# Optimization experiments

Measured on AMD Instinct MI355X. Metric: run time of the kernel, lower is better.

The kernel has to match this reference:

```python
import jax, jax.numpy as jnp
import numpy as np

N_EMBED = 1024
HEAD_SIZE = 128
B, T = 8, 2048


def setup_inputs() -> dict:
    key = jax.random.key(0)
    kx, kk, kq, kv = jax.random.split(key, 4)
    x = jax.random.normal(kx, (B, T, N_EMBED), dtype=jnp.float32)
    Wk = jax.random.normal(kk, (N_EMBED, HEAD_SIZE), dtype=jnp.float32) * (N_EMBED ** -0.5)
    Wq = jax.random.normal(kq, (N_EMBED, HEAD_SIZE), dtype=jnp.float32) * (N_EMBED ** -0.5)
    Wv = jax.random.normal(kv, (N_EMBED, HEAD_SIZE), dtype=jnp.float32) * (N_EMBED ** -0.5)
    return {"x": x, "Wk": Wk, "Wq": Wq, "Wv": Wv}


def reference(x, Wk, Wq, Wv):
    # x: [B, T, C]; single-head causal attention, dropout rate 0 (identity)
    t = x.shape[1]
    k = jnp.einsum("btc,ch->bth", x, Wk)  # keys
    q = jnp.einsum("btc,ch->bth", x, Wq)  # queries
    v = jnp.einsum("btc,ch->bth", x, Wv)  # values
    scale = k.shape[-1] ** -0.5
    scores = jnp.einsum("bqh,bkh->bqk", q, k) * scale  # [B, T, T]
    causal = jnp.tril(jnp.ones((t, t), dtype=bool))
    scores = jnp.where(causal, scores, -jnp.inf)
    attn = jax.nn.softmax(scores, axis=-1)
    return jnp.einsum("bqk,bkh->bqh", attn, v)
```

## Files before the change

### kernel.cpp

```cpp
#include <hip/hip_runtime.h>
#include <hip/hip_bf16.h>
#include <math.h>

#define B_ 8
#define T_ 2048
#define C_ 1024
#define D_ 128
#define M_ (B_*T_)

typedef __attribute__((ext_vector_type(8))) short short8;
typedef __attribute__((ext_vector_type(4))) float floatx4;
typedef __hip_bfloat16 bf16;

#define QSCALE 0.12751744416218247f

#define GLDS16(gsrc, ldst) \
    __builtin_amdgcn_global_load_lds((const __attribute__((address_space(1))) unsigned int*)(gsrc), \
                                     (__attribute__((address_space(3))) unsigned int*)(ldst), 16, 0, 0)

__global__ __launch_bounds__(256) void cvt_w3_kernel(const float* __restrict__ Wq,
                                                     const float* __restrict__ Wk,
                                                     const float* __restrict__ Wv,
                                                     bf16* __restrict__ Wt2) {
    __shared__ bf16 tl[64][136];
    const int t = threadIdx.x;
    const int kc = blockIdx.x, g = blockIdx.y;
    const int k0 = kc * 64;
    const float* W = (g == 0) ? Wq : (g == 1) ? Wk : Wv;
    {
        int k = t >> 2, n0 = (t & 3) * 32;
        const float* src = W + (size_t)(k0 + k) * 128 + n0;
#pragma unroll
        for (int j = 0; j < 4; ++j) {
            float4 v0 = *(const float4*)(src + j * 8);
            float4 v1 = *(const float4*)(src + j * 8 + 4);
            union { short8 s; __hip_bfloat162 h[4]; } u;
            __hip_bfloat162 h;
            h.x = __float2bfloat16(v0.x); h.y = __float2bfloat16(v0.y); u.h[0] = h;
            h.x = __float2bfloat16(v0.z); h.y = __float2bfloat16(v0.w); u.h[1] = h;
            h.x = __float2bfloat16(v1.x); h.y = __float2bfloat16(v1.y); u.h[2] = h;
            h.x = __float2bfloat16(v1.z); h.y = __float2bfloat16(v1.w); u.h[3] = h;
            *(short8*)&tl[k][n0 + j * 8] = u.s;
        }
    }
    __syncthreads();
    {
#pragma unroll
        for (int j = 0; j < 4; ++j) {
            int cid = t + j * 256;
            int lane = cid & 63, dk = (cid >> 6) & 1, cb = cid >> 7;
            int krow = dk * 32 + (lane >> 4) * 8;
            int ncol = cb * 16 + (lane & 15);
            union { short8 s; bf16 e[8]; } u;
#pragma unroll
            for (int e = 0; e < 8; ++e) u.e[e] = tl[krow + e][ncol];
            bf16* dst = Wt2 + ((((size_t)(g * 8 + cb) * 16 + kc) * 2 + dk) * 64 + lane) * 8;
            *(short8*)dst = u.s;
        }
    }
}

__global__ __launch_bounds__(256, 2) void proj13_kernel(const float* __restrict__ x,
                                                        const bf16* __restrict__ Wt2,
                                                        bf16* __restrict__ Qb,
                                                        bf16* __restrict__ Kb,
                                                        bf16* __restrict__ Vt) {
    __shared__ char smem[57344];
    bf16* wlds = (bf16*)smem;
    const int t = threadIdx.x;
    const int wave = t >> 6, lane = t & 63;
    const int quad = lane >> 4, l15 = lane & 15;
    const int wr = wave >> 1, wc = wave & 1;
    const int phys = blockIdx.x;
    const int lb = (phys & 7) * 64 + (phys >> 3);
    const int rt = lb >> 1, cg = lb & 1;
    const int row0 = rt * 64;

    const float* xsrc[4];
#pragma unroll
    for (int j = 0; j < 4; ++j)
        xsrc[j] = x + (size_t)(row0 + (wave * 4 + j) * 4 + quad) * 1024
                    + 4 * ((lane & 15) ^ ((j & 1) * 4 + quad));

    const bf16* wsrc[6];
#pragma unroll
    for (int j = 0; j < 6; ++j) {
        const int s = j * 4 + wave;
        const int chunkbase = (cg * 12 + (s >> 1)) * 32 + (s & 1);
        wsrc[j] = Wt2 + (size_t)chunkbase * 512 + lane * 8;
    }

    floatx4 acc[2][6];
#pragma unroll
    for (int m = 0; m < 2; ++m)
#pragma unroll
        for (int n = 0; n < 6; ++n) acc[m][n] = (floatx4)0.0f;

#pragma unroll
    for (int j = 0; j < 4; ++j)
        GLDS16(xsrc[j], smem + 24576 + (wave * 4 + j) * 1024);

    for (int kc = 0; kc < 16; ++kc) {
        __syncthreads();
#pragma unroll
        for (int j = 0; j < 6; ++j) {
            const int s = j * 4 + wave;
            GLDS16(wsrc[j] + kc * 1024, smem + s * 1024);
        }
        __syncthreads();
        if (kc < 15) {
            char* xd = smem + 24576 + ((kc + 1) & 1) * 16384;
#pragma unroll
            for (int j = 0; j < 4; ++j)
                GLDS16(xsrc[j] + (kc + 1) * 64, xd + (wave * 4 + j) * 1024);
        }
        const float* xb = (const float*)(smem + 24576 + (kc & 1) * 16384);
#pragma unroll
        for (int dk = 0; dk < 2; ++dk) {
            short8 af[2], bff[6];
#pragma unroll
            for (int m = 0; m < 2; ++m) {
                const int r = wr * 32 + m * 16 + l15;
                const int p0 = (dk * 32 + quad * 8) ^ ((l15 & 7) * 4);
                float4 a0 = *(const float4*)(xb + r * 64 + p0);
                float4 a1 = *(const float4*)(xb + r * 64 + (p0 ^ 4));
                union { short8 s; __hip_bfloat162 h[4]; } u;
                __hip_bfloat162 hh;
                hh.x = __float2bfloat16(a0.x); hh.y = __float2bfloat16(a0.y); u.h[0] = hh;
                hh.x = __float2bfloat16(a0.z); hh.y = __float2bfloat16(a0.w); u.h[1] = hh;
                hh.x = __float2bfloat16(a1.x); hh.y = __float2bfloat16(a1.y); u.h[2] = hh;
                hh.x = __float2bfloat16(a1.z); hh.y = __float2bfloat16(a1.w); u.h[3] = hh;
                af[m] = u.s;
            }
#pragma unroll
            for (int n = 0; n < 6; ++n) {
                const int c = wc * 6 + n;
                bff[n] = *(const short8*)(wlds + (size_t)(c * 2 + dk) * 512 + lane * 8);
            }
#pragma unroll
            for (int m = 0; m < 2; ++m)
#pragma unroll
                for (int n = 0; n < 6; ++n)
                    acc[m][n] = __builtin_amdgcn_mfma_f32_16x16x32_bf16(af[m], bff[n], acc[m][n], 0, 0, 0);
        }
    }

    __syncthreads();
    bf16* vtl = (bf16*)smem;
#pragma unroll
    for (int m = 0; m < 2; ++m)
#pragma unroll
        for (int r = 0; r < 4; ++r) {
            const int tt = wr * 32 + m * 16 + quad * 4 + r;
            const int row = row0 + tt;
#pragma unroll
            for (int n = 0; n < 6; ++n) {
                const int colb = cg * 192 + wc * 96 + n * 16;
                const int g = colb >> 7;
                const int lc = (colb & 127) + l15;
                const float v = acc[m][n][r];
                if (g == 0)      Qb[(size_t)row * 128 + lc] = __float2bfloat16(v * QSCALE);
                else if (g == 1) Kb[(size_t)row * 128 + lc] = __float2bfloat16(v);
                else             vtl[tt * 137 + lc] = __float2bfloat16(v);
            }
        }
    if (cg == 1) {
        __syncthreads();
        int d = t >> 1, toff = (t & 1) * 32;
        union { short8 s[4]; bf16 e[32]; } u;
#pragma unroll
        for (int i = 0; i < 32; ++i) u.e[i] = vtl[(toff + i) * 137 + d];
        int bb = row0 >> 11, t0 = row0 & 2047;
        bf16* dst = Vt + (size_t)(bb * D_ + d) * T_ + t0 + toff;
#pragma unroll
        for (int j = 0; j < 4; ++j) *(short8*)(dst + j * 8) = u.s[j];
    }
}

__global__ __launch_bounds__(256, 3) void flash_fm2_kernel(const bf16* __restrict__ Qb,
                                                           const bf16* __restrict__ Kb,
                                                           const bf16* __restrict__ Vt,
                                                           float* __restrict__ out,
                                                           bf16* __restrict__ Opart,
                                                           float* __restrict__ Lpart) {
    const int tile = blockIdx.x, seg = blockIdx.y, b = blockIdx.z;
    const int keys_total = (tile + 1) * 64;
    const int nseg = (keys_total + 255) >> 8;
    if (seg >= nseg) return;

    __shared__ bf16 lds_k[64][136];
    __shared__ bf16 lds_v[128][72];
    __shared__ bf16 lds_p[4][16][72];
    const int t = threadIdx.x;
    const int wave = t >> 6, lane = t & 63;
    const int quad = lane >> 4, l15 = lane & 15;
    const int q0 = tile * 64;
    const int k_start = seg << 8;
    const int k_end = min(k_start + 256, keys_total);
    const int nch = (k_end - k_start) >> 6;

    short8 qf[4];
    {
        int qm = q0 + wave * 16 + l15;
#pragma unroll
        for (int dk = 0; dk < 4; ++dk)
            qf[dk] = *(const short8*)(Qb + (size_t)(b * T_ + qm) * 128 + dk * 32 + quad * 8);
    }

    short8 kreg[4], vreg[4];
    {
        const int k0 = k_start;
#pragma unroll
        for (int j = 0; j < 4; ++j) {
            int c = t + j * 256;
            { int r = c >> 4, co = (c & 15) * 8;
              kreg[j] = *(const short8*)(Kb + (size_t)(b * T_ + k0 + r) * 128 + co); }
            { int d = c >> 3, co = (c & 7) * 8;
              vreg[j] = *(const short8*)(Vt + (size_t)b * (D_ * T_) + d * T_ + k0 + co); }
        }
    }

    floatx4 o_acc[8];
#pragma unroll
    for (int i = 0; i < 8; ++i) o_acc[i] = (floatx4)0.0f;
    float lp[4] = {0.f, 0.f, 0.f, 0.f};
    const int qrow = q0 + wave * 16 + quad * 4;

    for (int ch = 0; ch < nch; ++ch) {
        const int k0 = k_start + (ch << 6);
        __syncthreads();
#pragma unroll
        for (int j = 0; j < 4; ++j) {
            int c = t + j * 256;
            { int r = c >> 4, co = (c & 15) * 8; *(short8*)&lds_k[r][co] = kreg[j]; }
            { int d = c >> 3, co = (c & 7) * 8;  *(short8*)&lds_v[d][co] = vreg[j]; }
        }
        if (ch + 1 < nch) {
            const int kn = k0 + 64;
#pragma unroll
            for (int j = 0; j < 4; ++j) {
                int c = t + j * 256;
                { int r = c >> 4, co = (c & 15) * 8;
                  kreg[j] = *(const short8*)(Kb + (size_t)(b * T_ + kn + r) * 128 + co); }
                { int d = c >> 3, co = (c & 7) * 8;
                  vreg[j] = *(const short8*)(Vt + (size_t)b * (D_ * T_) + d * T_ + kn + co); }
            }
        }
        __syncthreads();

        floatx4 s[4];
#pragma unroll
        for (int nt = 0; nt < 4; ++nt) s[nt] = (floatx4)0.0f;
#pragma unroll
        for (int dk = 0; dk < 4; ++dk)
#pragma unroll
            for (int nt = 0; nt < 4; ++nt) {
                short8 kb = *(const short8*)&lds_k[nt * 16 + l15][dk * 32 + quad * 8];
                s[nt] = __builtin_amdgcn_mfma_f32_16x16x32_bf16(qf[dk], kb, s[nt], 0, 0, 0);
            }

        float sv[4][4];
#pragma unroll
        for (int nt = 0; nt < 4; ++nt)
#pragma unroll
            for (int r = 0; r < 4; ++r) sv[nt][r] = s[nt][r];

        if (k0 + 63 > q0) {
#pragma unroll
            for (int nt = 0; nt < 4; ++nt) {
                int key = k0 + nt * 16 + l15;
#pragma unroll
                for (int r = 0; r < 4; ++r)
                    if (key > qrow + r) sv[nt][r] = -1e30f;
            }
        }

#pragma unroll
        for (int nt = 0; nt < 4; ++nt)
#pragma unroll
            for (int r = 0; r < 4; ++r) sv[nt][r] = exp2f(sv[nt][r]);
#pragma unroll
        for (int r = 0; r < 4; ++r)
            lp[r] += (sv[0][r] + sv[1][r]) + (sv[2][r] + sv[3][r]);

#pragma unroll
        for (int nt = 0; nt < 4; ++nt)
#pragma unroll
            for (int r = 0; r < 4; ++r)
                lds_p[wave][quad * 4 + r][nt * 16 + l15] = __float2bfloat16(sv[nt][r]);
        short8 pa0 = *(const short8*)&lds_p[wave][l15][quad * 8];
        short8 pa1 = *(const short8*)&lds_p[wave][l15][32 + quad * 8];

#pragma unroll
        for (int nt = 0; nt < 8; ++nt) {
            short8 vb0 = *(const short8*)&lds_v[nt * 16 + l15][quad * 8];
            short8 vb1 = *(const short8*)&lds_v[nt * 16 + l15][32 + quad * 8];
            o_acc[nt] = __builtin_amdgcn_mfma_f32_16x16x32_bf16(pa0, vb0, o_acc[nt], 0, 0, 0);
            o_acc[nt] = __builtin_amdgcn_mfma_f32_16x16x32_bf16(pa1, vb1, o_acc[nt], 0, 0, 0);
        }
    }

    float l_i[4];
#pragma unroll
    for (int r = 0; r < 4; ++r) {
        float v = lp[r];
        v += __shfl_xor(v, 1);
        v += __shfl_xor(v, 2);
        v += __shfl_xor(v, 4);
        v += __shfl_xor(v, 8);
        l_i[r] = v;
    }

    const int lrow = wave * 16 + quad * 4;
    if (nseg == 1) {
        float inv_l[4];
#pragma unroll
        for (int r = 0; r < 4; ++r) inv_l[r] = 1.0f / l_i[r];
#pragma unroll
        for (int f = 0; f < 8; ++f)
#pragma unroll
            for (int r = 0; r < 4; ++r)
                out[(size_t)(b * T_ + qrow + r) * 128 + f * 16 + l15] = o_acc[f][r] * inv_l[r];
    } else {
        int pre = 0;
        for (int u = 4; u < tile; ++u) pre += (u + 4) >> 2;
        const size_t slot = (size_t)b * 140 + pre + seg;
        bf16* ob = Opart + slot * (64 * 128);
#pragma unroll
        for (int f = 0; f < 8; ++f)
#pragma unroll
            for (int r = 0; r < 4; ++r)
                ob[(size_t)(lrow + r) * 128 + f * 16 + l15] = __float2bfloat16(o_acc[f][r]);
        if (l15 == 0) {
#pragma unroll
            for (int r = 0; r < 4; ++r)
                Lpart[slot * 64 + lrow + r] = l_i[r];
        }
    }
}

__global__ __launch_bounds__(256) void combine4_kernel(const bf16* __restrict__ Opart,
                                                       const float* __restrict__ Lpart,
                                                       float* __restrict__ out) {
    const int tile = blockIdx.x + 4, b = blockIdx.y;
    const int nseg = (tile + 4) >> 2;
    int pre = 0;
    for (int u = 4; u < tile; ++u) pre += (u + 4) >> 2;
    const size_t slot0 = (size_t)b * 140 + pre;
    const int t = threadIdx.x;
    const int row = t >> 2, c0 = (t & 3) * 32;

    float lsum = 0.f;
    for (int j = 0; j < nseg; ++j) lsum += Lpart[(slot0 + j) * 64 + row];

    float acc[32];
#pragma unroll
    for (int i = 0; i < 32; ++i) acc[i] = 0.f;
    for (int j = 0; j < nseg; ++j) {
        const bf16* src = Opart + (slot0 + j) * (64 * 128) + (size_t)row * 128 + c0;
#pragma unroll
        for (int u = 0; u < 4; ++u) {
            short8 v8 = *(const short8*)(src + u * 8);
#pragma unroll
            for (int e = 0; e < 8; ++e) {
                union { unsigned int u32; float f; } cv;
                cv.u32 = ((unsigned int)(unsigned short)v8[e]) << 16;
                acc[u * 8 + e] += cv.f;
            }
        }
    }
    float inv = 1.0f / lsum;
    float* dst = out + (size_t)(b * T_ + tile * 64 + row) * 128 + c0;
#pragma unroll
    for (int i = 0; i < 32; ++i) dst[i] = acc[i] * inv;
}

extern "C" void kernel_launch(void* const* d_in, const int* in_sizes, int n_in,
                              void* d_out, int out_size, void* d_ws, size_t ws_size,
                              hipStream_t stream) {
    const float* x  = (const float*)d_in[0];
    const float* Wk = (const float*)d_in[1];
    const float* Wq = (const float*)d_in[2];
    const float* Wv = (const float*)d_in[3];
    float* out = (float*)d_out;

    char* ws = (char*)d_ws;
    bf16*  Wt2   = (bf16*)ws;
    bf16*  Qb    = (bf16*)(ws + 786432);
    bf16*  Kb    = (bf16*)(ws + 4980736);
    bf16*  Vt    = (bf16*)(ws + 9175040);
    bf16*  Opart = (bf16*)(ws + 13369344);
    float* Lpart = (float*)(ws + 31719424);

    cvt_w3_kernel<<<dim3(16, 3), 256, 0, stream>>>(Wq, Wk, Wv, Wt2);
    proj13_kernel<<<512, 256, 0, stream>>>(x, Wt2, Qb, Kb, Vt);
    flash_fm2_kernel<<<dim3(32, 8, B_), 256, 0, stream>>>(Qb, Kb, Vt, out, Opart, Lpart);
    combine4_kernel<<<dim3(28, B_), 256, 0, stream>>>(Opart, Lpart, out);
}
```

Baseline: 84.33 us.

## Convert x to bf16 once via registers and double-buffer weight tiles in projection

The projection kernel now loads x fp32 tiles into registers, converts them to bf16 once and stores them swizzled into LDS, instead of staging fp32 via global_load_lds and converting on every MFMA operand read. Weight tiles become double-buffered, with one barrier pair per k-chunk and explicit waitcnt/sched_barrier control, so the next chunk's loads overlap the current chunk's MFMAs. This cuts repeated conversion work and the LDS footprint of x. In exchange it raises LDS to 64KB, which may limit occupancy at two blocks per CU, and adds register pressure from prefetching x.

```diff
diff --git a/kernel.cpp b/kernel.cpp
--- a/kernel.cpp
+++ b/kernel.cpp
@@ -60,13 +60,12 @@
     }
 }
 
-__global__ __launch_bounds__(256, 2) void proj13_kernel(const float* __restrict__ x,
+__global__ __launch_bounds__(256, 2) void proj14_kernel(const float* __restrict__ x,
                                                         const bf16* __restrict__ Wt2,
                                                         bf16* __restrict__ Qb,
                                                         bf16* __restrict__ Kb,
                                                         bf16* __restrict__ Vt) {
-    __shared__ char smem[57344];
-    bf16* wlds = (bf16*)smem;
+    __shared__ __attribute__((aligned(16))) char smem[65536];
     const int t = threadIdx.x;
     const int wave = t >> 6, lane = t & 63;
     const int quad = lane >> 4, l15 = lane & 15;
@@ -76,12 +75,6 @@
     const int rt = lb >> 1, cg = lb & 1;
     const int row0 = rt * 64;
 
-    const float* xsrc[4];
-#pragma unroll
-    for (int j = 0; j < 4; ++j)
-        xsrc[j] = x + (size_t)(row0 + (wave * 4 + j) * 4 + quad) * 1024
-                    + 4 * ((lane & 15) ^ ((j & 1) * 4 + quad));
-
     const bf16* wsrc[6];
 #pragma unroll
     for (int j = 0; j < 6; ++j) {
@@ -90,60 +83,98 @@
         wsrc[j] = Wt2 + (size_t)chunkbase * 512 + lane * 8;
     }
 
+    const int xwrow = t >> 2;
+    const float* xbase = x + (size_t)(row0 + xwrow) * 1024 + (t & 3) * 16;
+    const int xwb0 = xwrow * 128 + (((t & 3) * 32) ^ ((xwrow & 7) << 4));
+    const int xwb1 = xwrow * 128 + ((((t & 3) * 32) + 16) ^ ((xwrow & 7) << 4));
+
     floatx4 acc[2][6];
 #pragma unroll
     for (int m = 0; m < 2; ++m)
 #pragma unroll
         for (int n = 0; n < 6; ++n) acc[m][n] = (floatx4)0.0f;
 
-#pragma unroll
-    for (int j = 0; j < 4; ++j)
-        GLDS16(xsrc[j], smem + 24576 + (wave * 4 + j) * 1024);
-
-    for (int kc = 0; kc < 16; ++kc) {
-        __syncthreads();
-#pragma unroll
-        for (int j = 0; j < 6; ++j) {
-            const int s = j * 4 + wave;
-            GLDS16(wsrc[j] + kc * 1024, smem + s * 1024);
-        }
-        __syncthreads();
-        if (kc < 15) {
-            char* xd = smem + 24576 + ((kc + 1) & 1) * 16384;
+    float4 xr[4];
+
+#define CVT_STORE_X(dstbase)                                                          \
+    {                                                                                 \
+        union { short8 s; __hip_bfloat162 h[4]; } u0, u1;                             \
+        __hip_bfloat162 h;                                                            \
+        h.x = __float2bfloat16(xr[0].x); h.y = __float2bfloat16(xr[0].y); u0.h[0] = h;\
+        h.x = __float2bfloat16(xr[0].z); h.y = __float2bfloat16(xr[0].w); u0.h[1] = h;\
+        h.x = __float2bfloat16(xr[1].x); h.y = __float2bfloat16(xr[1].y); u0.h[2] = h;\
+        h.x = __float2bfloat16(xr[1].z); h.y = __float2bfloat16(xr[1].w); u0.h[3] = h;\
+        h.x = __float2bfloat16(xr[2].x); h.y = __float2bfloat16(xr[2].y); u1.h[0] = h;\
+        h.x = __float2bfloat16(xr[2].z); h.y = __float2bfloat16(xr[2].w); u1.h[1] = h;\
+        h.x = __float2bfloat16(xr[3].x); h.y = __float2bfloat16(xr[3].y); u1.h[2] = h;\
+        h.x = __float2bfloat16(xr[3].z); h.y = __float2bfloat16(xr[3].w); u1.h[3] = h;\
+        *(short8*)((dstbase) + xwb0) = u0.s;                                          \
+        *(short8*)((dstbase) + xwb1) = u1.s;                                          \
+    }
+
+#define COMPUTE_KC(kc_)                                                               \
+    {                                                                                 \
+        const char* xb = smem + 49152 + ((kc_) & 1) * 8192;                           \
+        const char* wb = smem + ((kc_) & 1) * 24576;                                  \
+        _Pragma("unroll")                                                             \
+        for (int dk = 0; dk < 2; ++dk) {                                              \
+            short8 af[2], bff[6];                                                     \
+            _Pragma("unroll")                                                         \
+            for (int m = 0; m < 2; ++m) {                                             \
+                const int row = wr * 32 + m * 16 + l15;                               \
+                const int byt = row * 128 + ((dk * 64 + quad * 16) ^ ((row & 7) << 4));\
+                af[m] = *(const short8*)(xb + byt);                                   \
+            }                                                                         \
+            _Pragma("unroll")                                                         \
+            for (int n = 0; n < 6; ++n)                                               \
+                bff[n] = *(const short8*)(wb + (size_t)((wc * 6 + n) * 2 + dk) * 1024 \
+                                           + lane * 16);                              \
+            _Pragma("unroll")                                                         \
+            for (int m = 0; m < 2; ++m)                                               \
+                _Pragma("unroll")                                                     \
+                for (int n = 0; n < 6; ++n)                                           \
+                    acc[m][n] = __builtin_amdgcn_mfma_f32_16x16x32_bf16(af[m], bff[n],\
+                                                                  acc[m][n], 0, 0, 0);\
+        }                                                                             \
+    }
+
+#pragma unroll
+    for (int j = 0; j < 4; ++j) xr[j] = *(const float4*)(xbase + j * 4);
+    CVT_STORE_X(smem + 49152)
+#pragma unroll
+    for (int j = 0; j < 6; ++j)
+        GLDS16(wsrc[j], smem + (j * 4 + wave) * 1024);
+#pragma unroll
+    for (int j = 0; j < 4; ++j) xr[j] = *(const float4*)(xbase + 64 + j * 4);
+
+    for (int kc = 0; kc < 15; ++kc) {
+        __builtin_amdgcn_s_barrier();
+        {
+            char* wdst = smem + ((kc + 1) & 1) * 24576;
+            const size_t wko = (size_t)(kc + 1) * 1024;
+#pragma unroll
+            for (int j = 0; j < 6; ++j)
+                GLDS16(wsrc[j] + wko, wdst + (j * 4 + wave) * 1024);
+        }
+        CVT_STORE_X(smem + 49152 + ((kc + 1) & 1) * 8192)
+        if (kc < 14) {
 #pragma unroll
             for (int j = 0; j < 4; ++j)
-                GLDS16(xsrc[j] + (kc + 1) * 64, xd + (wave * 4 + j) * 1024);
-        }
-        const float* xb = (const float*)(smem + 24576 + (kc & 1) * 16384);
-#pragma unroll
-        for (int dk = 0; dk < 2; ++dk) {
-            short8 af[2], bff[6];
-#pragma unroll
-            for (int m = 0; m < 2; ++m) {
-                const int r = wr * 32 + m * 16 + l15;
-                const int p0 = (dk * 32 + quad * 8) ^ ((l15 & 7) * 4);
-                float4 a0 = *(const float4*)(xb + r * 64 + p0);
-                float4 a1 = *(const float4*)(xb + r * 64 + (p0 ^ 4));
-                union { short8 s; __hip_bfloat162 h[4]; } u;
-                __hip_bfloat162 hh;
-                hh.x = __float2bfloat16(a0.x); hh.y = __float2bfloat16(a0.y); u.h[0] = hh;
-                hh.x = __float2bfloat16(a0.z); hh.y = __float2bfloat16(a0.w); u.h[1] = hh;
-                hh.x = __float2bfloat16(a1.x); hh.y = __float2bfloat16(a1.y); u.h[2] = hh;
-                hh.x = __float2bfloat16(a1.z); hh.y = __float2bfloat16(a1.w); u.h[3] = hh;
-                af[m] = u.s;
-            }
-#pragma unroll
-            for (int n = 0; n < 6; ++n) {
-                const int c = wc * 6 + n;
-                bff[n] = *(const short8*)(wlds + (size_t)(c * 2 + dk) * 512 + lane * 8);
-            }
-#pragma unroll
-            for (int m = 0; m < 2; ++m)
-#pragma unroll
-                for (int n = 0; n < 6; ++n)
-                    acc[m][n] = __builtin_amdgcn_mfma_f32_16x16x32_bf16(af[m], bff[n], acc[m][n], 0, 0, 0);
-        }
-    }
+                xr[j] = *(const float4*)(xbase + (kc + 2) * 64 + j * 4);
+        }
+        asm volatile("s_waitcnt lgkmcnt(0)" ::: "memory");
+        __builtin_amdgcn_s_barrier();
+        __builtin_amdgcn_sched_barrier(0);
+        COMPUTE_KC(kc)
+    }
+    __builtin_amdgcn_s_barrier();
+    asm volatile("s_waitcnt vmcnt(0) lgkmcnt(0)" ::: "memory");
+    __builtin_amdgcn_s_barrier();
+    __builtin_amdgcn_sched_barrier(0);
+    COMPUTE_KC(15)
+
+#undef CVT_STORE_X
+#undef COMPUTE_KC
 
     __syncthreads();
     bf16* vtl = (bf16*)smem;
@@ -393,7 +424,7 @@
     float* Lpart = (float*)(ws + 31719424);
 
     cvt_w3_kernel<<<dim3(16, 3), 256, 0, stream>>>(Wq, Wk, Wv, Wt2);
-    proj13_kernel<<<512, 256, 0, stream>>>(x, Wt2, Qb, Kb, Vt);
+    proj14_kernel<<<512, 256, 0, stream>>>(x, Wt2, Qb, Kb, Vt);
     flash_fm2_kernel<<<dim3(32, 8, B_), 256, 0, stream>>>(Qb, Kb, Vt, out, Opart, Lpart);
     combine4_kernel<<<dim3(28, B_), 256, 0, stream>>>(Opart, Lpart, out);
 }
```

New measurement: 82.01 us. 1.03x faster.
